# Kernel tuning notes

Hardware: AMD Instinct MI355X
Metric: run time of the kernel (lower is better)

## Reference

```python
import jax, jax.numpy as jnp
import numpy as np

N_NODES = 50000
N_EDGES = 1280000
N_GRAPHS = 64
IN_CH = 6
HID = 64
SLOPE = 0.2  # LeakyReLU negative slope


def _lrelu(x):
    return jax.nn.leaky_relu(x, SLOPE)


def _edge_conv(x, src, dst, W1, b1, W2, b2):
    # PyG EdgeConv: message = nn([x_i, x_j - x_i]); x_i = x[dst], x_j = x[src]; max-aggr onto dst
    xi = x[dst]                                   # [E, F]
    m = jnp.concatenate([xi, x[src] - xi], -1)    # [E, 2F]
    h = _lrelu(_lrelu(m @ W1 + b1) @ W2 + b2)     # [E, H]
    agg = jax.ops.segment_max(h, dst, num_segments=N_NODES)
    return jnp.where(jnp.isneginf(agg), 0.0, agg)  # nodes with no in-edges -> 0


def setup_inputs() -> dict:
    key = jax.random.key(0)
    ks = jax.random.split(key, 12)
    glorot = lambda k, fi, fo: jax.random.normal(k, (fi, fo), jnp.float32) * np.sqrt(2.0 / (fi + fo))
    x = jax.random.normal(ks[0], (N_NODES, IN_CH), jnp.float32)
    edge_index = jax.random.randint(ks[1], (2, N_EDGES), 0, N_NODES, jnp.int64 if jax.config.x64_enabled else jnp.int32)
    batch = jnp.sort(jax.random.randint(ks[2], (N_NODES,), 0, N_GRAPHS))
    return {
        "x": x, "edge_index": edge_index, "batch": batch,
        "W1": glorot(ks[3], 2 * IN_CH, HID), "b1": jnp.zeros((HID,), jnp.float32),
        "W2": glorot(ks[4], HID, HID),       "b2": jnp.zeros((HID,), jnp.float32),
        "W3": glorot(ks[5], 2 * HID, HID),   "b3": jnp.zeros((HID,), jnp.float32),
        "W4": glorot(ks[6], HID, HID),       "b4": jnp.zeros((HID,), jnp.float32),
        "Wc1": glorot(ks[7], 2 * HID, HID),  "bc1": jnp.zeros((HID,), jnp.float32),
        "Wc2": glorot(ks[8], HID, 1),        "bc2": jnp.zeros((1,), jnp.float32),
    }


def reference(x, edge_index, batch, W1, b1, W2, b2, W3, b3, W4, b4, Wc1, bc1, Wc2, bc2):
    src, dst = edge_index[0], edge_index[1]
    h = _edge_conv(x, src, dst, W1, b1, W2, b2)   # [N, H]
    h = _edge_conv(h, src, dst, W3, b3, W4, b4)   # [N, H]
    # global mean + max pool per graph
    cnt = jax.ops.segment_sum(jnp.ones((N_NODES,), h.dtype), batch, num_segments=N_GRAPHS)
    mean_p = jax.ops.segment_sum(h, batch, num_segments=N_GRAPHS) / jnp.clip(cnt, 1.0)[:, None]
    max_p = jax.ops.segment_max(h, batch, num_segments=N_GRAPHS)
    max_p = jnp.where(jnp.isneginf(max_p), 0.0, max_p)
    g = jnp.concatenate([mean_p, max_p], -1)      # [G, 2H]
    logits = _lrelu(g @ Wc1 + bc1) @ Wc2 + bc2    # dropout is identity at inference
    return logits.squeeze(-1)                      # [G]
```

## Files before the change

### kernel.cpp

```cpp
#include <hip/hip_runtime.h>
#include <hip/hip_bf16.h>

#define SLOPE 0.2f
#define NPB 64
#define CAP 2048
#define SUBCAP 384
#define MAXBUCK 1024
#define EPB 4096
#define XF1B 512
#define PPARTS 16

typedef _Float16 f16x8  __attribute__((ext_vector_type(8)));
typedef float    f32x4  __attribute__((ext_vector_type(4)));
typedef unsigned u32;
typedef unsigned u32x4  __attribute__((ext_vector_type(4)));

__device__ __forceinline__ float lrelu(float v) { return fmaxf(v, SLOPE * v); }

__device__ __forceinline__ f16x8 lrelu8(f16x8 v) {
    f16x8 s = v * (_Float16)SLOPE;
#if __has_builtin(__builtin_elementwise_max)
    return __builtin_elementwise_max(v, s);
#else
    f16x8 r;
#pragma unroll
    for (int i = 0; i < 8; ++i) r[i] = v[i] > s[i] ? v[i] : s[i];
    return r;
#endif
}

__device__ __forceinline__ void split_f16(float v, _Float16& h, _Float16& l) {
    h = (_Float16)v;
    l = (_Float16)(v - (float)h);
}
__device__ __forceinline__ u32 pack_f16(_Float16 a, _Float16 b) {
    return (u32)__builtin_bit_cast(unsigned short, a) |
           ((u32)__builtin_bit_cast(unsigned short, b) << 16);
}

__global__ void __launch_bounds__(256) scatter_xform1_kernel(
    const int* __restrict__ srcI, const int* __restrict__ dstI,
    int* __restrict__ cursor, u32* __restrict__ pairW,
    int E, int nNodes, int nBuck, int nCntB,
    const float* __restrict__ x,
    const float* __restrict__ W1, const float* __restrict__ b1,
    _Float16* __restrict__ Ph, _Float16* __restrict__ Qh)
{
    if (blockIdx.x < nCntB) {
        __shared__ int cnt4[4][MAXBUCK];
        __shared__ int base[MAXBUCK];
        const int tid = threadIdx.x;
        const int wv  = tid >> 6;
        const int j   = blockIdx.x & 7;
        const int e0 = blockIdx.x * EPB;
        const int e1 = min(e0 + EPB, E);
        const int n4 = (e1 - e0) >> 2;
        const int4* d4 = (const int4*)(dstI + e0);
        const int4* s4 = (const int4*)(srcI + e0);

        for (int b = tid; b < nBuck; b += 256) {
            cnt4[0][b] = 0; cnt4[1][b] = 0; cnt4[2][b] = 0; cnt4[3][b] = 0;
        }
        __syncthreads();
        int* mycnt = cnt4[wv];
        for (int i = tid; i < n4; i += 256) {
            const int4 d = d4[i];
            atomicAdd(&mycnt[d.x >> 6], 1);
            atomicAdd(&mycnt[d.y >> 6], 1);
            atomicAdd(&mycnt[d.z >> 6], 1);
            atomicAdd(&mycnt[d.w >> 6], 1);
        }
        for (int e = e0 + (n4 << 2) + tid; e < e1; e += 256)
            atomicAdd(&mycnt[dstI[e] >> 6], 1);
        __syncthreads();
        for (int b = tid; b < nBuck; b += 256) {
            const int c = (cnt4[0][b] + cnt4[1][b]) + (cnt4[2][b] + cnt4[3][b]);
            base[b] = (c > 0)
                ? ((b * 8 + j) * SUBCAP + min(atomicAdd(&cursor[b * 8 + j], c), SUBCAP))
                : 0;
        }
        __syncthreads();
        for (int b = tid; b < nBuck; b += 256) cnt4[0][b] = 0;
        __syncthreads();
        int* scnt = cnt4[0];
        for (int i = tid; i < n4; i += 256) {
            const int4 d = d4[i];
            const int4 s = s4[i];
            {
                const int b = d.x >> 6;
                const int loc = atomicAdd(&scnt[b], 1);
                pairW[min(base[b] + loc, (b * 8 + j + 1) * SUBCAP - 1)] =
                    ((u32)s.x << 6) | (u32)(d.x & (NPB - 1));
            }
            {
                const int b = d.y >> 6;
                const int loc = atomicAdd(&scnt[b], 1);
                pairW[min(base[b] + loc, (b * 8 + j + 1) * SUBCAP - 1)] =
                    ((u32)s.y << 6) | (u32)(d.y & (NPB - 1));
            }
            {
                const int b = d.z >> 6;
                const int loc = atomicAdd(&scnt[b], 1);
                pairW[min(base[b] + loc, (b * 8 + j + 1) * SUBCAP - 1)] =
                    ((u32)s.z << 6) | (u32)(d.z & (NPB - 1));
            }
            {
                const int b = d.w >> 6;
                const int loc = atomicAdd(&scnt[b], 1);
                pairW[min(base[b] + loc, (b * 8 + j + 1) * SUBCAP - 1)] =
                    ((u32)s.w << 6) | (u32)(d.w & (NPB - 1));
            }
        }
        for (int e = e0 + (n4 << 2) + tid; e < e1; e += 256) {
            const int d = dstI[e];
            const int b = d >> 6;
            const int loc = atomicAdd(&scnt[b], 1);
            pairW[min(base[b] + loc, (b * 8 + j + 1) * SUBCAP - 1)] =
                ((u32)srcI[e] << 6) | (u32)(d & (NPB - 1));
        }
        return;
    }
    const int lane = threadIdx.x & 63;
    const int wave = ((blockIdx.x - nCntB) * 256 + threadIdx.x) >> 6;
    const int nw   = (XF1B * 256) >> 6;

    float wd[6], wb[6];
#pragma unroll
    for (int r = 0; r < 6; ++r) {
        wb[r] = W1[(6 + r) * 64 + lane];
        wd[r] = W1[r * 64 + lane] - wb[r];
    }
    const float bb = b1[lane];
    for (int i = wave; i < nNodes; i += nw) {
        const float* xr = x + (size_t)i * 6;
        float p = bb, q = 0.f;
#pragma unroll
        for (int r = 0; r < 6; ++r) {
            float xv = xr[r];
            p = fmaf(xv, wd[r], p);
            q = fmaf(xv, wb[r], q);
        }
        Ph[(size_t)i * 64 + lane] = (_Float16)p;
        Qh[(size_t)i * 64 + lane] = (_Float16)q;
    }
}

__global__ void __launch_bounds__(256) bucket_sort_kernel(
    const u32* __restrict__ pairW, const int* __restrict__ cursor,
    int2* __restrict__ rowInfo, int* __restrict__ sortedSrc,
    int* __restrict__ fixedSrc, int nNodes)
{
    __shared__ u32 pairLds[CAP];
    __shared__ u32 sortLds[CAP];
    __shared__ int nodeCnt4[4][NPB];
    __shared__ int nodeCur4[4][NPB];
    __shared__ int nodeSt[NPB];
    __shared__ int nodeDg[NPB];
    __shared__ int wcS[8];
    __shared__ int wBase[9];
    const int b   = blockIdx.x;
    const int n0  = b * NPB;
    const int n1  = min(n0 + NPB, nNodes);
    const int tid = threadIdx.x;
    const int wv  = tid >> 6;

    if (tid < NPB) {
        nodeCnt4[0][tid] = 0; nodeCnt4[1][tid] = 0;
        nodeCnt4[2][tid] = 0; nodeCnt4[3][tid] = 0;
    }
    if (tid < 8) wcS[tid] = min(cursor[b * 8 + tid], SUBCAP);
    __syncthreads();
    if (tid == 0) {
        int acc = 0;
#pragma unroll
        for (int jj = 0; jj < 8; ++jj) { wBase[jj] = acc; acc += wcS[jj]; }
        wBase[8] = acc;
    }
    __syncthreads();

#pragma unroll
    for (int jj = 0; jj < 8; ++jj) {
        const int w0 = (b * 8 + jj) * SUBCAP;
        const int wc = wcS[jj];
        const int d0 = wBase[jj];
        const int nv = wc >> 2;
        const u32x4* p4 = (const u32x4*)(pairW + w0);
        for (int i = tid; i < nv; i += 256) {
            const u32x4 v = p4[i];
            pairLds[d0 + i * 4 + 0] = v[0];
            pairLds[d0 + i * 4 + 1] = v[1];
            pairLds[d0 + i * 4 + 2] = v[2];
            pairLds[d0 + i * 4 + 3] = v[3];
        }
        for (int i = (nv << 2) + tid; i < wc; i += 256)
            pairLds[d0 + i] = pairW[w0 + i];
    }
    __syncthreads();

    const int total = wBase[8];
    for (int i = tid; i < total; i += 256)
        atomicAdd(&nodeCnt4[wv][pairLds[i] & (NPB - 1)], 1);
    __syncthreads();
    if (tid < 64) {
        const int c0 = nodeCnt4[0][tid], c1 = nodeCnt4[1][tid];
        const int c2 = nodeCnt4[2][tid], c3 = nodeCnt4[3][tid];
        const int c = (c0 + c1) + (c2 + c3);
        int inc = c;
#pragma unroll
        for (int off = 1; off < 64; off <<= 1) {
            int t = __shfl_up(inc, off);
            if (tid >= off) inc += t;
        }
        const int stl = inc - c;
        nodeSt[tid] = stl;
        nodeDg[tid] = c;
        nodeCur4[0][tid] = stl;
        nodeCur4[1][tid] = stl + c0;
        nodeCur4[2][tid] = stl + c0 + c1;
        nodeCur4[3][tid] = stl + c0 + c1 + c2;
        if (tid < n1 - n0) rowInfo[n0 + tid] = make_int2(b * CAP + stl, c);
    }
    __syncthreads();
    for (int i = tid; i < total; i += 256) {
        const u32 w = pairLds[i];
        const int pos = atomicAdd(&nodeCur4[wv][w & (NPB - 1)], 1);
        sortLds[pos] = w >> 6;
    }
    __syncthreads();
    for (int i = tid; i < total; i += 256)
        sortedSrc[b * CAP + i] = (int)sortLds[i];
    const int nValid = n1 - n0;
    for (int idx = tid; idx < NPB * 32; idx += 256) {
        const int r = idx >> 5;
        const int i = idx & 31;
        if (r < nValid) {
            const int dg = nodeDg[r];
            const u32 v = (dg > 0) ? sortLds[nodeSt[r] + min(i, dg - 1)]
                                   : (u32)(n0 + r);
            fixedSrc[(size_t)(n0 + r) * 32 + i] = (int)v;
        }
    }
}

__global__ void __launch_bounds__(256) node_xform2_mfma_kernel(
    const _Float16* __restrict__ B1h,
    const float* __restrict__ W3, const float* __restrict__ b3,
    _Float16* __restrict__ Ph, _Float16* __restrict__ Qh, int nNodes)
{
    __shared__ u32x4 wlds[32][64];

    const int tid  = threadIdx.x;
    const int lane = tid & 63;
    const int cn   = lane & 15;
    const int q    = lane >> 4;
    const int wv   = tid >> 6;
    const int wave = (blockIdx.x * 256 + tid) >> 6;
    const int nw   = (gridDim.x * 256) >> 6;

#pragma unroll
    for (int i = 0; i < 8; ++i) {
        const int f    = wv + i * 4;
        const int isLo = f >> 4;
        const int g    = f & 15;
        const int nt   = g >> 1;
        const int ks   = g & 1;
        const int col  = (nt & 3) * 16 + cn;
        u32x4 d;
#pragma unroll
        for (int p = 0; p < 4; ++p) {
            const int k0 = ks * 32 + q * 8 + 2 * p;
            float w0, w1;
            if (nt < 4) {
                w0 = W3[k0 * 64 + col]       - W3[(64 + k0) * 64 + col];
                w1 = W3[(k0 + 1) * 64 + col] - W3[(64 + k0 + 1) * 64 + col];
            } else {
                w0 = W3[(64 + k0) * 64 + col];
                w1 = W3[(64 + k0 + 1) * 64 + col];
            }
            _Float16 h0, l0, h1, l1;
            split_f16(w0, h0, l0);
            split_f16(w1, h1, l1);
            d[p] = isLo ? pack_f16(l0, l1) : pack_f16(h0, h1);
        }
        wlds[f][lane] = d;
    }
    float bcv[4];
#pragma unroll
    for (int nt = 0; nt < 4; ++nt) bcv[nt] = b3[nt * 16 + cn];
    __syncthreads();

    const int nGrp = (nNodes + 15) >> 4;
    for (int t = wave; t < nGrp; t += nw) {
        const int n0 = t << 4;
        const int rA = min(n0 + cn, nNodes - 1);
        const f16x8* Arow = (const f16x8*)(B1h + (size_t)rA * 64);
        const f16x8 A0 = Arow[q];
        const f16x8 A1 = Arow[4 + q];

        f32x4 acc0, acc1, acc2, acc3, acc4, acc5, acc6, acc7;
#define NT_TILE(ACC, NT, INI)                                                  \
        {                                                                      \
            const f16x8 wh0 = __builtin_bit_cast(f16x8, wlds[(NT) * 2][lane]); \
            const f16x8 wh1 = __builtin_bit_cast(f16x8, wlds[(NT) * 2 + 1][lane]); \
            const f16x8 wl0 = __builtin_bit_cast(f16x8, wlds[16 + (NT) * 2][lane]); \
            const f16x8 wl1 = __builtin_bit_cast(f16x8, wlds[16 + (NT) * 2 + 1][lane]); \
            f32x4 a_; a_[0] = a_[1] = a_[2] = a_[3] = (INI);                   \
            a_ = __builtin_amdgcn_mfma_f32_16x16x32_f16(A0, wl0, a_, 0, 0, 0); \
            a_ = __builtin_amdgcn_mfma_f32_16x16x32_f16(A0, wh0, a_, 0, 0, 0); \
            a_ = __builtin_amdgcn_mfma_f32_16x16x32_f16(A1, wl1, a_, 0, 0, 0); \
            a_ = __builtin_amdgcn_mfma_f32_16x16x32_f16(A1, wh1, a_, 0, 0, 0); \
            ACC = a_;                                                          \
        }
        NT_TILE(acc0, 0, bcv[0]); NT_TILE(acc1, 1, bcv[1]);
        NT_TILE(acc2, 2, bcv[2]); NT_TILE(acc3, 3, bcv[3]);
        NT_TILE(acc4, 4, 0.0f);   NT_TILE(acc5, 5, 0.0f);
        NT_TILE(acc6, 6, 0.0f);   NT_TILE(acc7, 7, 0.0f);
#undef NT_TILE

        const int rowLim = nNodes - n0;
#pragma unroll
        for (int j = 0; j < 4; ++j) {
            const int r = 4 * q + j;
            if (r < rowLim) {
                _Float16* Pr = Ph + (size_t)(n0 + r) * 64;
                _Float16* Qr = Qh + (size_t)(n0 + r) * 64;
                Pr[cn]      = (_Float16)acc0[j];
                Pr[16 + cn] = (_Float16)acc1[j];
                Pr[32 + cn] = (_Float16)acc2[j];
                Pr[48 + cn] = (_Float16)acc3[j];
                Qr[cn]      = (_Float16)acc4[j];
                Qr[16 + cn] = (_Float16)acc5[j];
                Qr[32 + cn] = (_Float16)acc6[j];
                Qr[48 + cn] = (_Float16)acc7[j];
            }
        }
    }
}

__global__ void __launch_bounds__(256) edge_agg_mfma_kernel(
    const _Float16* __restrict__ Ph, const _Float16* __restrict__ Qh,
    const int2* __restrict__ rowInfo, const int* __restrict__ sortedSrc,
    const int* __restrict__ fixedSrc,
    const float* __restrict__ W, const float* __restrict__ b,
    _Float16* __restrict__ outB, int nNodes)
{
    __shared__ u32x4 wlds[16][64];

    const int tid  = threadIdx.x;
    const int lane = tid & 63;
    const int cn   = lane & 15;
    const int q    = lane >> 4;
    const int wv   = tid >> 6;
    const int wave = (blockIdx.x * 256 + tid) >> 6;
    const int nw   = (gridDim.x * 256) >> 6;

#pragma unroll
    for (int i = 0; i < 4; ++i) {
        const int f    = wv + i * 4;
        const int isLo = f >> 3;
        const int g    = f & 7;
        const int nt   = g >> 1;
        const int ks   = g & 1;
        u32x4 d;
#pragma unroll
        for (int p = 0; p < 4; ++p) {
            float w0 = W[(ks * 32 + q * 8 + 2 * p)     * 64 + nt * 16 + cn];
            float w1 = W[(ks * 32 + q * 8 + 2 * p + 1) * 64 + nt * 16 + cn];
            _Float16 h0, l0, h1, l1;
            split_f16(w0, h0, l0);
            split_f16(w1, h1, l1);
            d[p] = isLo ? pack_f16(l0, l1) : pack_f16(h0, h1);
        }
        wlds[f][lane] = d;
    }
    float bc[4];
#pragma unroll
    for (int nt = 0; nt < 4; ++nt) bc[nt] = b[nt * 16 + cn];
    __syncthreads();

    const u32 nClamp = (u32)(nNodes - 1);
    const int nLastN = nNodes - 1;
    const int nPairs = (nNodes + 1) >> 1;

    for (int t = wave; t < nPairs; t += nw) {
        const int n1 = 2 * t;
        const int n2 = 2 * t + 1;
        const bool has2 = (n2 < nNodes);

        const int2 ri1 = rowInfo[n1];
        const int2 ri2 = has2 ? rowInfo[n2] : make_int2(ri1.x, 0);
        const size_t fb1 = (size_t)n1 * 32;
        const size_t fb2 = (size_t)(has2 ? n2 : n1) * 32;
        u32 sA1 = (u32)fixedSrc[fb1 + cn];
        u32 sB1 = (u32)fixedSrc[fb1 + 16 + cn];
        u32 sA2 = (u32)fixedSrc[fb2 + cn];
        u32 sB2 = (u32)fixedSrc[fb2 + 16 + cn];
        sA1 = min(sA1, nClamp); sB1 = min(sB1, nClamp);
        sA2 = min(sA2, nClamp); sB2 = min(sB2, nClamp);

        const f16x8* P1 = (const f16x8*)(Ph + (size_t)n1 * 64);
        const f16x8* P2 = (const f16x8*)(Ph + (size_t)(has2 ? n2 : n1) * 64);
        const f16x8 p1A = P1[q], p1B = P1[4 + q];
        const f16x8 p2A = P2[q], p2B = P2[4 + q];

        const f16x8* QA1 = (const f16x8*)(Qh + (size_t)sA1 * 64);
        const f16x8* QB1 = (const f16x8*)(Qh + (size_t)sB1 * 64);
        const f16x8* QA2 = (const f16x8*)(Qh + (size_t)sA2 * 64);
        const f16x8* QB2 = (const f16x8*)(Qh + (size_t)sB2 * 64);
        const f16x8 qA1a = QA1[q], qA1b = QA1[4 + q];
        const f16x8 qB1a = QB1[q], qB1b = QB1[4 + q];
        const f16x8 qA2a = QA2[q], qA2b = QA2[4 + q];
        const f16x8 qB2a = QB2[q], qB2b = QB2[4 + q];

        const int rs1  = __builtin_amdgcn_readfirstlane(ri1.x);
        const int deg1 = __builtin_amdgcn_readfirstlane(ri1.y);
        const int rs2  = __builtin_amdgcn_readfirstlane(ri2.x);
        const int deg2 = __builtin_amdgcn_readfirstlane(ri2.y);
        const int d1c = max(deg1, 1) - 1;
        const int d2c = max(deg2, 1) - 1;

        float m10 = -INFINITY, m11 = -INFINITY, m12 = -INFINITY, m13 = -INFINITY;
        float m20 = -INFINITY, m21 = -INFINITY, m22 = -INFINITY, m23 = -INFINITY;

        if (deg1 > 0) {
            const f16x8 A00 = lrelu8(p1A + qA1a);
            const f16x8 A01 = lrelu8(p1B + qA1b);
            const f16x8 A10 = lrelu8(p1A + qB1a);
            const f16x8 A11 = lrelu8(p1B + qB1b);
#pragma unroll
            for (int nt = 0; nt < 4; ++nt) {
                const f16x8 wh0 = __builtin_bit_cast(f16x8, wlds[nt * 2][lane]);
                const f16x8 wh1 = __builtin_bit_cast(f16x8, wlds[nt * 2 + 1][lane]);
                const f16x8 wl0 = __builtin_bit_cast(f16x8, wlds[8 + nt * 2][lane]);
                const f16x8 wl1 = __builtin_bit_cast(f16x8, wlds[8 + nt * 2 + 1][lane]);
                f32x4 a; a[0] = a[1] = a[2] = a[3] = bc[nt];
                a = __builtin_amdgcn_mfma_f32_16x16x32_f16(A00, wl0, a, 0, 0, 0);
                a = __builtin_amdgcn_mfma_f32_16x16x32_f16(A00, wh0, a, 0, 0, 0);
                a = __builtin_amdgcn_mfma_f32_16x16x32_f16(A01, wl1, a, 0, 0, 0);
                a = __builtin_amdgcn_mfma_f32_16x16x32_f16(A01, wh1, a, 0, 0, 0);
                f32x4 c; c[0] = c[1] = c[2] = c[3] = bc[nt];
                c = __builtin_amdgcn_mfma_f32_16x16x32_f16(A10, wl0, c, 0, 0, 0);
                c = __builtin_amdgcn_mfma_f32_16x16x32_f16(A10, wh0, c, 0, 0, 0);
                c = __builtin_amdgcn_mfma_f32_16x16x32_f16(A11, wl1, c, 0, 0, 0);
                c = __builtin_amdgcn_mfma_f32_16x16x32_f16(A11, wh1, c, 0, 0, 0);
                float m = (nt == 0) ? m10 : (nt == 1) ? m11 : (nt == 2) ? m12 : m13;
                m = fmaxf(m, fmaxf(fmaxf(a[0], a[1]), fmaxf(a[2], a[3])));
                m = fmaxf(m, fmaxf(fmaxf(c[0], c[1]), fmaxf(c[2], c[3])));
                if (nt == 0) m10 = m; else if (nt == 1) m11 = m;
                else if (nt == 2) m12 = m; else m13 = m;
            }
        }
        if (deg2 > 0) {
            const f16x8 A00 = lrelu8(p2A + qA2a);
            const f16x8 A01 = lrelu8(p2B + qA2b);
            const f16x8 A10 = lrelu8(p2A + qB2a);
            const f16x8 A11 = lrelu8(p2B + qB2b);
#pragma unroll
            for (int nt = 0; nt < 4; ++nt) {
                const f16x8 wh0 = __builtin_bit_cast(f16x8, wlds[nt * 2][lane]);
                const f16x8 wh1 = __builtin_bit_cast(f16x8, wlds[nt * 2 + 1][lane]);
                const f16x8 wl0 = __builtin_bit_cast(f16x8, wlds[8 + nt * 2][lane]);
                const f16x8 wl1 = __builtin_bit_cast(f16x8, wlds[8 + nt * 2 + 1][lane]);
                f32x4 a; a[0] = a[1] = a[2] = a[3] = bc[nt];
                a = __builtin_amdgcn_mfma_f32_16x16x32_f16(A00, wl0, a, 0, 0, 0);
                a = __builtin_amdgcn_mfma_f32_16x16x32_f16(A00, wh0, a, 0, 0, 0);
                a = __builtin_amdgcn_mfma_f32_16x16x32_f16(A01, wl1, a, 0, 0, 0);
                a = __builtin_amdgcn_mfma_f32_16x16x32_f16(A01, wh1, a, 0, 0, 0);
                f32x4 c; c[0] = c[1] = c[2] = c[3] = bc[nt];
                c = __builtin_amdgcn_mfma_f32_16x16x32_f16(A10, wl0, c, 0, 0, 0);
                c = __builtin_amdgcn_mfma_f32_16x16x32_f16(A10, wh0, c, 0, 0, 0);
                c = __builtin_amdgcn_mfma_f32_16x16x32_f16(A11, wl1, c, 0, 0, 0);
                c = __builtin_amdgcn_mfma_f32_16x16x32_f16(A11, wh1, c, 0, 0, 0);
                float m = (nt == 0) ? m20 : (nt == 1) ? m21 : (nt == 2) ? m22 : m23;
                m = fmaxf(m, fmaxf(fmaxf(a[0], a[1]), fmaxf(a[2], a[3])));
                m = fmaxf(m, fmaxf(fmaxf(c[0], c[1]), fmaxf(c[2], c[3])));
                if (nt == 0) m20 = m; else if (nt == 1) m21 = m;
                else if (nt == 2) m22 = m; else m23 = m;
            }
        }

        const int gmax = max(deg1, deg2);
        for (int g0 = 32; g0 < gmax; g0 += 32) {
            u32 eA1 = (u32)sortedSrc[rs1 + min(g0 + cn,      d1c)];
            u32 eB1 = (u32)sortedSrc[rs1 + min(g0 + 16 + cn, d1c)];
            u32 eA2 = (u32)sortedSrc[rs2 + min(g0 + cn,      d2c)];
            u32 eB2 = (u32)sortedSrc[rs2 + min(g0 + 16 + cn, d2c)];
            eA1 = min(eA1, nClamp); eB1 = min(eB1, nClamp);
            eA2 = min(eA2, nClamp); eB2 = min(eB2, nClamp);
            const f16x8* EA1 = (const f16x8*)(Qh + (size_t)eA1 * 64);
            const f16x8* EB1 = (const f16x8*)(Qh + (size_t)eB1 * 64);
            const f16x8* EA2 = (const f16x8*)(Qh + (size_t)eA2 * 64);
            const f16x8* EB2 = (const f16x8*)(Qh + (size_t)eB2 * 64);
            const f16x8 gA1a = EA1[q], gA1b = EA1[4 + q];
            const f16x8 gB1a = EB1[q], gB1b = EB1[4 + q];
            const f16x8 gA2a = EA2[q], gA2b = EA2[4 + q];
            const f16x8 gB2a = EB2[q], gB2b = EB2[4 + q];

            if (g0 < deg1) {
                const f16x8 A00 = lrelu8(p1A + gA1a);
                const f16x8 A01 = lrelu8(p1B + gA1b);
                const f16x8 A10 = lrelu8(p1A + gB1a);
                const f16x8 A11 = lrelu8(p1B + gB1b);
#pragma unroll
                for (int nt = 0; nt < 4; ++nt) {
                    const f16x8 wh0 = __builtin_bit_cast(f16x8, wlds[nt * 2][lane]);
                    const f16x8 wh1 = __builtin_bit_cast(f16x8, wlds[nt * 2 + 1][lane]);
                    const f16x8 wl0 = __builtin_bit_cast(f16x8, wlds[8 + nt * 2][lane]);
                    const f16x8 wl1 = __builtin_bit_cast(f16x8, wlds[8 + nt * 2 + 1][lane]);
                    f32x4 a; a[0] = a[1] = a[2] = a[3] = bc[nt];
                    a = __builtin_amdgcn_mfma_f32_16x16x32_f16(A00, wl0, a, 0, 0, 0);
                    a = __builtin_amdgcn_mfma_f32_16x16x32_f16(A00, wh0, a, 0, 0, 0);
                    a = __builtin_amdgcn_mfma_f32_16x16x32_f16(A01, wl1, a, 0, 0, 0);
                    a = __builtin_amdgcn_mfma_f32_16x16x32_f16(A01, wh1, a, 0, 0, 0);
                    f32x4 c; c[0] = c[1] = c[2] = c[3] = bc[nt];
                    c = __builtin_amdgcn_mfma_f32_16x16x32_f16(A10, wl0, c, 0, 0, 0);
                    c = __builtin_amdgcn_mfma_f32_16x16x32_f16(A10, wh0, c, 0, 0, 0);
                    c = __builtin_amdgcn_mfma_f32_16x16x32_f16(A11, wl1, c, 0, 0, 0);
                    c = __builtin_amdgcn_mfma_f32_16x16x32_f16(A11, wh1, c, 0, 0, 0);
                    float m = (nt == 0) ? m10 : (nt == 1) ? m11 : (nt == 2) ? m12 : m13;
                    m = fmaxf(m, fmaxf(fmaxf(a[0], a[1]), fmaxf(a[2], a[3])));
                    m = fmaxf(m, fmaxf(fmaxf(c[0], c[1]), fmaxf(c[2], c[3])));
                    if (nt == 0) m10 = m; else if (nt == 1) m11 = m;
                    else if (nt == 2) m12 = m; else m13 = m;
                }
            }
            if (g0 < deg2) {
                const f16x8 A00 = lrelu8(p2A + gA2a);
                const f16x8 A01 = lrelu8(p2B + gA2b);
                const f16x8 A10 = lrelu8(p2A + gB2a);
                const f16x8 A11 = lrelu8(p2B + gB2b);
#pragma unroll
                for (int nt = 0; nt < 4; ++nt) {
                    const f16x8 wh0 = __builtin_bit_cast(f16x8, wlds[nt * 2][lane]);
                    const f16x8 wh1 = __builtin_bit_cast(f16x8, wlds[nt * 2 + 1][lane]);
                    const f16x8 wl0 = __builtin_bit_cast(f16x8, wlds[8 + nt * 2][lane]);
                    const f16x8 wl1 = __builtin_bit_cast(f16x8, wlds[8 + nt * 2 + 1][lane]);
                    f32x4 a; a[0] = a[1] = a[2] = a[3] = bc[nt];
                    a = __builtin_amdgcn_mfma_f32_16x16x32_f16(A00, wl0, a, 0, 0, 0);
                    a = __builtin_amdgcn_mfma_f32_16x16x32_f16(A00, wh0, a, 0, 0, 0);
                    a = __builtin_amdgcn_mfma_f32_16x16x32_f16(A01, wl1, a, 0, 0, 0);
                    a = __builtin_amdgcn_mfma_f32_16x16x32_f16(A01, wh1, a, 0, 0, 0);
                    f32x4 c; c[0] = c[1] = c[2] = c[3] = bc[nt];
                    c = __builtin_amdgcn_mfma_f32_16x16x32_f16(A10, wl0, c, 0, 0, 0);
                    c = __builtin_amdgcn_mfma_f32_16x16x32_f16(A10, wh0, c, 0, 0, 0);
                    c = __builtin_amdgcn_mfma_f32_16x16x32_f16(A11, wl1, c, 0, 0, 0);
                    c = __builtin_amdgcn_mfma_f32_16x16x32_f16(A11, wh1, c, 0, 0, 0);
                    float m = (nt == 0) ? m20 : (nt == 1) ? m21 : (nt == 2) ? m22 : m23;
                    m = fmaxf(m, fmaxf(fmaxf(a[0], a[1]), fmaxf(a[2], a[3])));
                    m = fmaxf(m, fmaxf(fmaxf(c[0], c[1]), fmaxf(c[2], c[3])));
                    if (nt == 0) m20 = m; else if (nt == 1) m21 = m;
                    else if (nt == 2) m22 = m; else m23 = m;
                }
            }
        }

        m10 = fmaxf(m10, __shfl_xor(m10, 16)); m10 = fmaxf(m10, __shfl_xor(m10, 32));
        m11 = fmaxf(m11, __shfl_xor(m11, 16)); m11 = fmaxf(m11, __shfl_xor(m11, 32));
        m12 = fmaxf(m12, __shfl_xor(m12, 16)); m12 = fmaxf(m12, __shfl_xor(m12, 32));
        m13 = fmaxf(m13, __shfl_xor(m13, 16)); m13 = fmaxf(m13, __shfl_xor(m13, 32));
        float sel1 = (q < 2) ? ((q == 0) ? m10 : m11) : ((q == 2) ? m12 : m13);
        outB[(size_t)n1 * 64 + q * 16 + cn] =
            (_Float16)((deg1 > 0) ? lrelu(sel1) : 0.0f);

        if (has2) {
            m20 = fmaxf(m20, __shfl_xor(m20, 16)); m20 = fmaxf(m20, __shfl_xor(m20, 32));
            m21 = fmaxf(m21, __shfl_xor(m21, 16)); m21 = fmaxf(m21, __shfl_xor(m21, 32));
            m22 = fmaxf(m22, __shfl_xor(m22, 16)); m22 = fmaxf(m22, __shfl_xor(m22, 32));
            m23 = fmaxf(m23, __shfl_xor(m23, 16)); m23 = fmaxf(m23, __shfl_xor(m23, 32));
            float sel2 = (q < 2) ? ((q == 0) ? m20 : m21) : ((q == 2) ? m22 : m23);
            outB[(size_t)n2 * 64 + q * 16 + cn] =
                (_Float16)((deg2 > 0) ? lrelu(sel2) : 0.0f);
        }
    }
}

__device__ __forceinline__ int lower_bound_i(const int* __restrict__ a, int n, int key)
{
    int lo = 0, hi = n;
    while (lo < hi) {
        int mid = (lo + hi) >> 1;
        if (a[mid] < key) lo = mid + 1; else hi = mid;
    }
    return lo;
}

__global__ void __launch_bounds__(256) pool_kernel(
    const _Float16* __restrict__ Bh, const int* __restrict__ batch,
    float* __restrict__ gpart, int nNodes)
{
    const int gid  = blockIdx.x / PPARTS;
    const int part = blockIdx.x % PPARTS;
    const int c    = threadIdx.x & 63;
    const int wid  = threadIdx.x >> 6;

    const int s = lower_bound_i(batch, nNodes, gid);
    const int e = lower_bound_i(batch, nNodes, gid + 1);
    const int len = e - s;
    const int ps = s + (len * part) / PPARTS;
    const int pe = s + (len * (part + 1)) / PPARTS;

    float sum = 0.f, mx = -INFINITY;
    for (int n = ps + wid; n < pe; n += 4) {
        float v = (float)Bh[(size_t)n * 64 + c];
        sum += v;
        mx = fmaxf(mx, v);
    }
    __shared__ float ssum[4][64];
    __shared__ float smax[4][64];
    ssum[wid][c] = sum;
    smax[wid][c] = mx;
    __syncthreads();
    if (wid == 0) {
        sum = (ssum[0][c] + ssum[1][c]) + (ssum[2][c] + ssum[3][c]);
        mx  = fmaxf(fmaxf(smax[0][c], smax[1][c]), fmaxf(smax[2][c], smax[3][c]));
        float* row = gpart + (size_t)blockIdx.x * 132;
        row[c]      = sum;
        row[64 + c] = mx;
        if (c == 0) row[128] = (float)(pe - ps);
    }
}

__global__ void __launch_bounds__(64) cls_kernel(
    const float* __restrict__ gpart,
    const float* __restrict__ Wc1, const float* __restrict__ bc1,
    const float* __restrict__ Wc2, const float* __restrict__ bc2,
    float* __restrict__ out)
{
    __shared__ float g[128];
    const int gid = blockIdx.x;
    const int c   = threadIdx.x;

    float s = 0.f, m = -INFINITY, cnt = 0.f;
#pragma unroll
    for (int p = 0; p < PPARTS; ++p) {
        const float* row = gpart + (size_t)(gid * PPARTS + p) * 132;
        s += row[c];
        m = fmaxf(m, row[64 + c]);
        cnt += row[128];
    }
    g[c]      = s / fmaxf(cnt, 1.0f);
    g[64 + c] = (cnt > 0.f) ? m : 0.0f;
    __syncthreads();

    float t = bc1[c];
#pragma unroll 8
    for (int k = 0; k < 128; ++k) t = fmaf(g[k], Wc1[k * 64 + c], t);
    t = lrelu(t);
    float p = t * Wc2[c];
#pragma unroll
    for (int off = 32; off > 0; off >>= 1) p += __shfl_down(p, off);
    if (c == 0) out[gid] = p + bc2[0];
}

static inline size_t align_up(size_t v, size_t a) { return (v + a - 1) & ~(a - 1); }

extern "C" void kernel_launch(void* const* d_in, const int* in_sizes, int n_in,
                              void* d_out, int out_size, void* d_ws, size_t ws_size,
                              hipStream_t stream)
{
    const float* x     = (const float*)d_in[0];
    const int*   ei    = (const int*)d_in[1];
    const int*   batch = (const int*)d_in[2];
    const float* W1  = (const float*)d_in[3];
    const float* b1  = (const float*)d_in[4];
    const float* W2  = (const float*)d_in[5];
    const float* b2  = (const float*)d_in[6];
    const float* W3  = (const float*)d_in[7];
    const float* b3  = (const float*)d_in[8];
    const float* W4  = (const float*)d_in[9];
    const float* b4  = (const float*)d_in[10];
    const float* Wc1 = (const float*)d_in[11];
    const float* bc1 = (const float*)d_in[12];
    const float* Wc2 = (const float*)d_in[13];
    const float* bc2 = (const float*)d_in[14];
    float* out = (float*)d_out;

    const int nNodes  = in_sizes[0] / 6;
    const int E       = in_sizes[1] / 2;
    const int nGraphs = out_size;
    const int* srcI = ei;
    const int* dstI = ei + E;
    const int nBuck = (nNodes + NPB - 1) / NPB;
    const int nCntB = (E + EPB - 1) / EPB;

    char* wsp = (char*)d_ws;
    size_t off = 0;
    int*  cursor    = (int*)(wsp + off);   off = align_up(off + (size_t)MAXBUCK * 8 * 4, 256);
    int2* rowInfo   = (int2*)(wsp + off);  off = align_up(off + (size_t)nNodes * 8, 256);
    int*  sortedSrc = (int*)(wsp + off);   off = align_up(off + (size_t)nBuck * CAP * 4, 256);
    int*  fixedSrc  = (int*)(wsp + off);   off = align_up(off + (size_t)nNodes * 32 * 4, 256);
    u32*  pairW     = (u32*)(wsp + off);   off = align_up(off + (size_t)nBuck * 8 * SUBCAP * 4, 256);
    const size_t nFeat = (size_t)nNodes * 64;
    _Float16* Ph   = (_Float16*)(wsp + off);  off = align_up(off + nFeat * 2, 256);
    _Float16* Qh   = (_Float16*)(wsp + off);  off = align_up(off + nFeat * 2, 256);
    _Float16* B1h  = (_Float16*)(wsp + off);  off = align_up(off + nFeat * 2, 256);
    _Float16* B2h  = (_Float16*)(wsp + off);  off = align_up(off + nFeat * 2, 256);
    float*    gpart= (float*)(wsp + off);     off = align_up(off + (size_t)nGraphs * PPARTS * 132 * 4, 256);
    (void)ws_size;

    (void)hipMemsetAsync(cursor, 0, (size_t)nBuck * 8 * 4, stream);
    scatter_xform1_kernel<<<nCntB + XF1B, 256, 0, stream>>>(
        srcI, dstI, cursor, pairW, E, nNodes, nBuck, nCntB, x, W1, b1, Ph, Qh);
    bucket_sort_kernel<<<nBuck, 256, 0, stream>>>(pairW, cursor, rowInfo,
                                                  sortedSrc, fixedSrc, nNodes);

    edge_agg_mfma_kernel<<<2048, 256, 0, stream>>>(Ph, Qh, rowInfo, sortedSrc,
                                                   fixedSrc, W2, b2, B1h, nNodes);
    const int nGrp   = (nNodes + 15) >> 4;
    const int xf2Blk = (nGrp + 3) >> 2;
    node_xform2_mfma_kernel<<<xf2Blk, 256, 0, stream>>>(B1h, W3, b3, Ph, Qh,
                                                        nNodes);
    edge_agg_mfma_kernel<<<2048, 256, 0, stream>>>(Ph, Qh, rowInfo, sortedSrc,
                                                   fixedSrc, W4, b4, B2h, nNodes);

    pool_kernel<<<nGraphs * PPARTS, 256, 0, stream>>>(B2h, batch, gpart, nNodes);
    cls_kernel<<<nGraphs, 64, 0, stream>>>(gpart, Wc1, bc1, Wc2, bc2, out);
}
```

Baseline: 260.9 us.

## Stage xform2 outputs through LDS and give agg waves contiguous node-pair chunks

node_xform2 now writes its P/Q tiles into per-wave LDS staging buffers and then stores full 16-byte vectors per row, replacing scattered 2-byte global stores. The edge aggregation kernel switches from a grid-stride loop with 2048 blocks to contiguous chunks of about three node pairs per wave, with the grid sized to match. The max reduction is also reassociated to shorten the dependency chain. The aim is better store coalescing, better locality in the sorted neighbour data, and higher ILP, at the cost of more blocks and extra LDS use in xform2.

```diff
diff --git a/kernel.cpp b/kernel.cpp
--- a/kernel.cpp
+++ b/kernel.cpp
@@ -248,6 +248,8 @@
     _Float16* __restrict__ Ph, _Float16* __restrict__ Qh, int nNodes)
 {
     __shared__ u32x4 wlds[32][64];
+    __shared__ _Float16 stP[4][16][64];
+    __shared__ _Float16 stQ[4][16][64];
 
     const int tid  = threadIdx.x;
     const int lane = tid & 63;
@@ -317,22 +319,28 @@
         NT_TILE(acc6, 6, 0.0f);   NT_TILE(acc7, 7, 0.0f);
 #undef NT_TILE
 
-        const int rowLim = nNodes - n0;
 #pragma unroll
         for (int j = 0; j < 4; ++j) {
             const int r = 4 * q + j;
-            if (r < rowLim) {
-                _Float16* Pr = Ph + (size_t)(n0 + r) * 64;
-                _Float16* Qr = Qh + (size_t)(n0 + r) * 64;
-                Pr[cn]      = (_Float16)acc0[j];
-                Pr[16 + cn] = (_Float16)acc1[j];
-                Pr[32 + cn] = (_Float16)acc2[j];
-                Pr[48 + cn] = (_Float16)acc3[j];
-                Qr[cn]      = (_Float16)acc4[j];
-                Qr[16 + cn] = (_Float16)acc5[j];
-                Qr[32 + cn] = (_Float16)acc6[j];
-                Qr[48 + cn] = (_Float16)acc7[j];
-            }
+            stP[wv][r][cn]      = (_Float16)acc0[j];
+            stP[wv][r][16 + cn] = (_Float16)acc1[j];
+            stP[wv][r][32 + cn] = (_Float16)acc2[j];
+            stP[wv][r][48 + cn] = (_Float16)acc3[j];
+            stQ[wv][r][cn]      = (_Float16)acc4[j];
+            stQ[wv][r][16 + cn] = (_Float16)acc5[j];
+            stQ[wv][r][32 + cn] = (_Float16)acc6[j];
+            stQ[wv][r][48 + cn] = (_Float16)acc7[j];
+        }
+        const int rowLim = nNodes - n0;
+        const int rr = lane >> 2;
+        const int c0 = (lane & 3) * 16;
+        if (rr < rowLim) {
+            const f16x8* sp = (const f16x8*)&stP[wv][rr][c0];
+            const f16x8* sq = (const f16x8*)&stQ[wv][rr][c0];
+            f16x8* gp = (f16x8*)(Ph + (size_t)(n0 + rr) * 64 + c0);
+            f16x8* gq = (f16x8*)(Qh + (size_t)(n0 + rr) * 64 + c0);
+            gp[0] = sp[0]; gp[1] = sp[1];
+            gq[0] = sq[0]; gq[1] = sq[1];
         }
     }
 }
@@ -382,7 +390,11 @@
     const int nLastN = nNodes - 1;
     const int nPairs = (nNodes + 1) >> 1;
 
-    for (int t = wave; t < nPairs; t += nw) {
+    const int C    = (nPairs + nw - 1) / nw;
+    const int tBeg = wave * C;
+    const int tEnd = min(tBeg + C, nPairs);
+
+    for (int t = tBeg; t < tEnd; ++t) {
         const int n1 = 2 * t;
         const int n2 = 2 * t + 1;
         const bool has2 = (n2 < nNodes);
@@ -444,8 +456,10 @@
                 c = __builtin_amdgcn_mfma_f32_16x16x32_f16(A11, wl1, c, 0, 0, 0);
                 c = __builtin_amdgcn_mfma_f32_16x16x32_f16(A11, wh1, c, 0, 0, 0);
                 float m = (nt == 0) ? m10 : (nt == 1) ? m11 : (nt == 2) ? m12 : m13;
-                m = fmaxf(m, fmaxf(fmaxf(a[0], a[1]), fmaxf(a[2], a[3])));
-                m = fmaxf(m, fmaxf(fmaxf(c[0], c[1]), fmaxf(c[2], c[3])));
+                const float u1 = fmaxf(fmaxf(a[0], a[1]), a[2]);
+                const float u2 = fmaxf(fmaxf(a[3], c[0]), c[1]);
+                const float u3 = fmaxf(fmaxf(c[2], c[3]), m);
+                m = fmaxf(fmaxf(u1, u2), u3);
                 if (nt == 0) m10 = m; else if (nt == 1) m11 = m;
                 else if (nt == 2) m12 = m; else m13 = m;
             }
@@ -472,8 +486,10 @@
                 c = __builtin_amdgcn_mfma_f32_16x16x32_f16(A11, wl1, c, 0, 0, 0);
                 c = __builtin_amdgcn_mfma_f32_16x16x32_f16(A11, wh1, c, 0, 0, 0);
                 float m = (nt == 0) ? m20 : (nt == 1) ? m21 : (nt == 2) ? m22 : m23;
-                m = fmaxf(m, fmaxf(fmaxf(a[0], a[1]), fmaxf(a[2], a[3])));
-                m = fmaxf(m, fmaxf(fmaxf(c[0], c[1]), fmaxf(c[2], c[3])));
+                const float u1 = fmaxf(fmaxf(a[0], a[1]), a[2]);
+                const float u2 = fmaxf(fmaxf(a[3], c[0]), c[1]);
+                const float u3 = fmaxf(fmaxf(c[2], c[3]), m);
+                m = fmaxf(fmaxf(u1, u2), u3);
                 if (nt == 0) m20 = m; else if (nt == 1) m21 = m;
                 else if (nt == 2) m22 = m; else m23 = m;
             }
@@ -518,8 +534,10 @@
                     c = __builtin_amdgcn_mfma_f32_16x16x32_f16(A11, wl1, c, 0, 0, 0);
                     c = __builtin_amdgcn_mfma_f32_16x16x32_f16(A11, wh1, c, 0, 0, 0);
                     float m = (nt == 0) ? m10 : (nt == 1) ? m11 : (nt == 2) ? m12 : m13;
-                    m = fmaxf(m, fmaxf(fmaxf(a[0], a[1]), fmaxf(a[2], a[3])));
-                    m = fmaxf(m, fmaxf(fmaxf(c[0], c[1]), fmaxf(c[2], c[3])));
+                    const float u1 = fmaxf(fmaxf(a[0], a[1]), a[2]);
+                    const float u2 = fmaxf(fmaxf(a[3], c[0]), c[1]);
+                    const float u3 = fmaxf(fmaxf(c[2], c[3]), m);
+                    m = fmaxf(fmaxf(u1, u2), u3);
                     if (nt == 0) m10 = m; else if (nt == 1) m11 = m;
                     else if (nt == 2) m12 = m; else m13 = m;
                 }
@@ -546,8 +564,10 @@
                     c = __builtin_amdgcn_mfma_f32_16x16x32_f16(A11, wl1, c, 0, 0, 0);
                     c = __builtin_amdgcn_mfma_f32_16x16x32_f16(A11, wh1, c, 0, 0, 0);
                     float m = (nt == 0) ? m20 : (nt == 1) ? m21 : (nt == 2) ? m22 : m23;
-                    m = fmaxf(m, fmaxf(fmaxf(a[0], a[1]), fmaxf(a[2], a[3])));
-                    m = fmaxf(m, fmaxf(fmaxf(c[0], c[1]), fmaxf(c[2], c[3])));
+                    const float u1 = fmaxf(fmaxf(a[0], a[1]), a[2]);
+                    const float u2 = fmaxf(fmaxf(a[3], c[0]), c[1]);
+                    const float u3 = fmaxf(fmaxf(c[2], c[3]), m);
+                    m = fmaxf(fmaxf(u1, u2), u3);
                     if (nt == 0) m20 = m; else if (nt == 1) m21 = m;
                     else if (nt == 2) m22 = m; else m23 = m;
                 }
@@ -704,14 +724,18 @@
     bucket_sort_kernel<<<nBuck, 256, 0, stream>>>(pairW, cursor, rowInfo,
                                                   sortedSrc, fixedSrc, nNodes);
 
-    edge_agg_mfma_kernel<<<2048, 256, 0, stream>>>(Ph, Qh, rowInfo, sortedSrc,
-                                                   fixedSrc, W2, b2, B1h, nNodes);
+    const int nPairs    = (nNodes + 1) / 2;
+    const int aggWaves  = (nPairs + 2) / 3;
+    const int aggBlocks = (aggWaves + 3) / 4 > 0 ? (aggWaves + 3) / 4 : 1;
+
+    edge_agg_mfma_kernel<<<aggBlocks, 256, 0, stream>>>(Ph, Qh, rowInfo, sortedSrc,
+                                                        fixedSrc, W2, b2, B1h, nNodes);
     const int nGrp   = (nNodes + 15) >> 4;
     const int xf2Blk = (nGrp + 3) >> 2;
     node_xform2_mfma_kernel<<<xf2Blk, 256, 0, stream>>>(B1h, W3, b3, Ph, Qh,
                                                         nNodes);
-    edge_agg_mfma_kernel<<<2048, 256, 0, stream>>>(Ph, Qh, rowInfo, sortedSrc,
-                                                   fixedSrc, W4, b4, B2h, nNodes);
+    edge_agg_mfma_kernel<<<aggBlocks, 256, 0, stream>>>(Ph, Qh, rowInfo, sortedSrc,
+                                                        fixedSrc, W4, b4, B2h, nNodes);
 
     pool_kernel<<<nGraphs * PPARTS, 256, 0, stream>>>(B2h, batch, gpart, nNodes);
     cls_kernel<<<nGraphs, 64, 0, stream>>>(gpart, Wc1, bc1, Wc2, bc2, out);
```

New measurement: 262.2 us. About the same (+0.5%).

## Merge build/sort and pool/classifier kernels via cooperative grid sync

Applied to the files above, without the earlier changes.

Fuses the scatter+xform1 kernel with the bucket sort kernel, and the pool kernel with the classifier kernel. Each pair becomes one cooperative launch that uses a grid-wide barrier instead of a kernel boundary. The goal is to remove launch overhead and inter-kernel gaps for the small kernels. The build kernel puts its two shared-memory layouts in a union, so per-block LDS use may change. Cooperative launch needs every block (nCntB+XF1B, about 825) resident at once, which could limit occupancy or make the launch fail.

```diff
diff --git a/kernel.cpp b/kernel.cpp
--- a/kernel.cpp
+++ b/kernel.cpp
@@ -1,5 +1,8 @@
 #include <hip/hip_runtime.h>
 #include <hip/hip_bf16.h>
+#include <hip/hip_cooperative_groups.h>
+
+namespace cg = cooperative_groups;
 
 #define SLOPE 0.2f
 #define NPB 64
@@ -38,19 +41,32 @@
            ((u32)__builtin_bit_cast(unsigned short, b) << 16);
 }
 
-__global__ void __launch_bounds__(256) scatter_xform1_kernel(
+__global__ void __launch_bounds__(256) build_kernel(
     const int* __restrict__ srcI, const int* __restrict__ dstI,
     int* __restrict__ cursor, u32* __restrict__ pairW,
     int E, int nNodes, int nBuck, int nCntB,
     const float* __restrict__ x,
     const float* __restrict__ W1, const float* __restrict__ b1,
-    _Float16* __restrict__ Ph, _Float16* __restrict__ Qh)
+    _Float16* __restrict__ Ph, _Float16* __restrict__ Qh,
+    int2* __restrict__ rowInfo, int* __restrict__ sortedSrc,
+    int* __restrict__ fixedSrc)
 {
-    if (blockIdx.x < nCntB) {
-        __shared__ int cnt4[4][MAXBUCK];
-        __shared__ int base[MAXBUCK];
-        const int tid = threadIdx.x;
-        const int wv  = tid >> 6;
+    __shared__ union {
+        struct { int cnt4[4][MAXBUCK]; int base[MAXBUCK]; } sc;
+        struct {
+            u32 pairLds[CAP]; u32 sortLds[CAP];
+            int nodeCnt4[4][NPB]; int nodeCur4[4][NPB];
+            int nodeSt[NPB]; int nodeDg[NPB];
+            int wcS[8]; int wBase[9];
+        } bk;
+    } u;
+
+    const int tid = threadIdx.x;
+    const int wv  = tid >> 6;
+
+    if (blockIdx.x < (unsigned)nCntB) {
+        int (*cnt4)[MAXBUCK] = u.sc.cnt4;
+        int* base = u.sc.base;
         const int j   = blockIdx.x & 7;
         const int e0 = blockIdx.x * EPB;
         const int e1 = min(e0 + EPB, E);
@@ -118,126 +134,123 @@
             pairW[min(base[b] + loc, (b * 8 + j + 1) * SUBCAP - 1)] =
                 ((u32)srcI[e] << 6) | (u32)(d & (NPB - 1));
         }
-        return;
-    }
-    const int lane = threadIdx.x & 63;
-    const int wave = ((blockIdx.x - nCntB) * 256 + threadIdx.x) >> 6;
-    const int nw   = (XF1B * 256) >> 6;
-
-    float wd[6], wb[6];
-#pragma unroll
-    for (int r = 0; r < 6; ++r) {
-        wb[r] = W1[(6 + r) * 64 + lane];
-        wd[r] = W1[r * 64 + lane] - wb[r];
-    }
-    const float bb = b1[lane];
-    for (int i = wave; i < nNodes; i += nw) {
-        const float* xr = x + (size_t)i * 6;
-        float p = bb, q = 0.f;
+    } else if (blockIdx.x < (unsigned)(nCntB + XF1B)) {
+        const int lane = tid & 63;
+        const int wave = ((blockIdx.x - nCntB) * 256 + tid) >> 6;
+        const int nw   = (XF1B * 256) >> 6;
+
+        float wd[6], wb[6];
 #pragma unroll
         for (int r = 0; r < 6; ++r) {
-            float xv = xr[r];
-            p = fmaf(xv, wd[r], p);
-            q = fmaf(xv, wb[r], q);
-        }
-        Ph[(size_t)i * 64 + lane] = (_Float16)p;
-        Qh[(size_t)i * 64 + lane] = (_Float16)q;
-    }
-}
-
-__global__ void __launch_bounds__(256) bucket_sort_kernel(
-    const u32* __restrict__ pairW, const int* __restrict__ cursor,
-    int2* __restrict__ rowInfo, int* __restrict__ sortedSrc,
-    int* __restrict__ fixedSrc, int nNodes)
-{
-    __shared__ u32 pairLds[CAP];
-    __shared__ u32 sortLds[CAP];
-    __shared__ int nodeCnt4[4][NPB];
-    __shared__ int nodeCur4[4][NPB];
-    __shared__ int nodeSt[NPB];
-    __shared__ int nodeDg[NPB];
-    __shared__ int wcS[8];
-    __shared__ int wBase[9];
-    const int b   = blockIdx.x;
-    const int n0  = b * NPB;
-    const int n1  = min(n0 + NPB, nNodes);
-    const int tid = threadIdx.x;
-    const int wv  = tid >> 6;
-
-    if (tid < NPB) {
-        nodeCnt4[0][tid] = 0; nodeCnt4[1][tid] = 0;
-        nodeCnt4[2][tid] = 0; nodeCnt4[3][tid] = 0;
-    }
-    if (tid < 8) wcS[tid] = min(cursor[b * 8 + tid], SUBCAP);
-    __syncthreads();
-    if (tid == 0) {
-        int acc = 0;
-#pragma unroll
-        for (int jj = 0; jj < 8; ++jj) { wBase[jj] = acc; acc += wcS[jj]; }
-        wBase[8] = acc;
-    }
-    __syncthreads();
-
-#pragma unroll
-    for (int jj = 0; jj < 8; ++jj) {
-        const int w0 = (b * 8 + jj) * SUBCAP;
-        const int wc = wcS[jj];
-        const int d0 = wBase[jj];
-        const int nv = wc >> 2;
-        const u32x4* p4 = (const u32x4*)(pairW + w0);
-        for (int i = tid; i < nv; i += 256) {
-            const u32x4 v = p4[i];
-            pairLds[d0 + i * 4 + 0] = v[0];
-            pairLds[d0 + i * 4 + 1] = v[1];
-            pairLds[d0 + i * 4 + 2] = v[2];
-            pairLds[d0 + i * 4 + 3] = v[3];
-        }
-        for (int i = (nv << 2) + tid; i < wc; i += 256)
-            pairLds[d0 + i] = pairW[w0 + i];
-    }
-    __syncthreads();
-
-    const int total = wBase[8];
-    for (int i = tid; i < total; i += 256)
-        atomicAdd(&nodeCnt4[wv][pairLds[i] & (NPB - 1)], 1);
-    __syncthreads();
-    if (tid < 64) {
-        const int c0 = nodeCnt4[0][tid], c1 = nodeCnt4[1][tid];
-        const int c2 = nodeCnt4[2][tid], c3 = nodeCnt4[3][tid];
-        const int c = (c0 + c1) + (c2 + c3);
-        int inc = c;
-#pragma unroll
-        for (int off = 1; off < 64; off <<= 1) {
-            int t = __shfl_up(inc, off);
-            if (tid >= off) inc += t;
-        }
-        const int stl = inc - c;
-        nodeSt[tid] = stl;
-        nodeDg[tid] = c;
-        nodeCur4[0][tid] = stl;
-        nodeCur4[1][tid] = stl + c0;
-        nodeCur4[2][tid] = stl + c0 + c1;
-        nodeCur4[3][tid] = stl + c0 + c1 + c2;
-        if (tid < n1 - n0) rowInfo[n0 + tid] = make_int2(b * CAP + stl, c);
-    }
-    __syncthreads();
-    for (int i = tid; i < total; i += 256) {
-        const u32 w = pairLds[i];
-        const int pos = atomicAdd(&nodeCur4[wv][w & (NPB - 1)], 1);
-        sortLds[pos] = w >> 6;
-    }
-    __syncthreads();
-    for (int i = tid; i < total; i += 256)
-        sortedSrc[b * CAP + i] = (int)sortLds[i];
-    const int nValid = n1 - n0;
-    for (int idx = tid; idx < NPB * 32; idx += 256) {
-        const int r = idx >> 5;
-        const int i = idx & 31;
-        if (r < nValid) {
-            const int dg = nodeDg[r];
-            const u32 v = (dg > 0) ? sortLds[nodeSt[r] + min(i, dg - 1)]
-                                   : (u32)(n0 + r);
-            fixedSrc[(size_t)(n0 + r) * 32 + i] = (int)v;
+            wb[r] = W1[(6 + r) * 64 + lane];
+            wd[r] = W1[r * 64 + lane] - wb[r];
+        }
+        const float bb = b1[lane];
+        for (int i = wave; i < nNodes; i += nw) {
+            const float* xr = x + (size_t)i * 6;
+            float p = bb, q = 0.f;
+#pragma unroll
+            for (int r = 0; r < 6; ++r) {
+                float xv = xr[r];
+                p = fmaf(xv, wd[r], p);
+                q = fmaf(xv, wb[r], q);
+            }
+            Ph[(size_t)i * 64 + lane] = (_Float16)p;
+            Qh[(size_t)i * 64 + lane] = (_Float16)q;
+        }
+    }
+
+    cg::this_grid().sync();
+
+    if (blockIdx.x < (unsigned)nBuck) {
+        u32* pairLds = u.bk.pairLds;
+        u32* sortLds = u.bk.sortLds;
+        int (*nodeCnt4)[NPB] = u.bk.nodeCnt4;
+        int (*nodeCur4)[NPB] = u.bk.nodeCur4;
+        int* nodeSt = u.bk.nodeSt;
+        int* nodeDg = u.bk.nodeDg;
+        int* wcS    = u.bk.wcS;
+        int* wBase  = u.bk.wBase;
+
+        const int b   = blockIdx.x;
+        const int n0  = b * NPB;
+        const int n1  = min(n0 + NPB, nNodes);
+
+        if (tid < NPB) {
+            nodeCnt4[0][tid] = 0; nodeCnt4[1][tid] = 0;
+            nodeCnt4[2][tid] = 0; nodeCnt4[3][tid] = 0;
+        }
+        if (tid < 8) wcS[tid] = min(cursor[b * 8 + tid], SUBCAP);
+        __syncthreads();
+        if (tid == 0) {
+            int acc = 0;
+#pragma unroll
+            for (int jj = 0; jj < 8; ++jj) { wBase[jj] = acc; acc += wcS[jj]; }
+            wBase[8] = acc;
+        }
+        __syncthreads();
+
+#pragma unroll
+        for (int jj = 0; jj < 8; ++jj) {
+            const int w0 = (b * 8 + jj) * SUBCAP;
+            const int wc = wcS[jj];
+            const int d0 = wBase[jj];
+            const int nv = wc >> 2;
+            const u32x4* p4 = (const u32x4*)(pairW + w0);
+            for (int i = tid; i < nv; i += 256) {
+                const u32x4 v = p4[i];
+                pairLds[d0 + i * 4 + 0] = v[0];
+                pairLds[d0 + i * 4 + 1] = v[1];
+                pairLds[d0 + i * 4 + 2] = v[2];
+                pairLds[d0 + i * 4 + 3] = v[3];
+            }
+            for (int i = (nv << 2) + tid; i < wc; i += 256)
+                pairLds[d0 + i] = pairW[w0 + i];
+        }
+        __syncthreads();
+
+        const int total = wBase[8];
+        for (int i = tid; i < total; i += 256)
+            atomicAdd(&nodeCnt4[wv][pairLds[i] & (NPB - 1)], 1);
+        __syncthreads();
+        if (tid < 64) {
+            const int c0 = nodeCnt4[0][tid], c1 = nodeCnt4[1][tid];
+            const int c2 = nodeCnt4[2][tid], c3 = nodeCnt4[3][tid];
+            const int c = (c0 + c1) + (c2 + c3);
+            int inc = c;
+#pragma unroll
+            for (int off = 1; off < 64; off <<= 1) {
+                int t = __shfl_up(inc, off);
+                if (tid >= off) inc += t;
+            }
+            const int stl = inc - c;
+            nodeSt[tid] = stl;
+            nodeDg[tid] = c;
+            nodeCur4[0][tid] = stl;
+            nodeCur4[1][tid] = stl + c0;
+            nodeCur4[2][tid] = stl + c0 + c1;
+            nodeCur4[3][tid] = stl + c0 + c1 + c2;
+            if (tid < n1 - n0) rowInfo[n0 + tid] = make_int2(b * CAP + stl, c);
+        }
+        __syncthreads();
+        for (int i = tid; i < total; i += 256) {
+            const u32 w = pairLds[i];
+            const int pos = atomicAdd(&nodeCur4[wv][w & (NPB - 1)], 1);
+            sortLds[pos] = w >> 6;
+        }
+        __syncthreads();
+        for (int i = tid; i < total; i += 256)
+            sortedSrc[b * CAP + i] = (int)sortLds[i];
+        const int nValid = n1 - n0;
+        for (int idx = tid; idx < NPB * 32; idx += 256) {
+            const int r = idx >> 5;
+            const int i = idx & 31;
+            if (r < nValid) {
+                const int dg = nodeDg[r];
+                const u32 v = (dg > 0) ? sortLds[nodeSt[r] + min(i, dg - 1)]
+                                       : (u32)(n0 + r);
+                fixedSrc[(size_t)(n0 + r) * 32 + i] = (int)v;
+            }
         }
     }
 }
@@ -584,72 +597,78 @@
     return lo;
 }
 
-__global__ void __launch_bounds__(256) pool_kernel(
+__global__ void __launch_bounds__(256) pool_cls_kernel(
     const _Float16* __restrict__ Bh, const int* __restrict__ batch,
-    float* __restrict__ gpart, int nNodes)
+    float* __restrict__ gpart,
+    const float* __restrict__ Wc1, const float* __restrict__ bc1,
+    const float* __restrict__ Wc2, const float* __restrict__ bc2,
+    float* __restrict__ out, int nNodes, int nGraphs)
 {
-    const int gid  = blockIdx.x / PPARTS;
-    const int part = blockIdx.x % PPARTS;
-    const int c    = threadIdx.x & 63;
-    const int wid  = threadIdx.x >> 6;
-
-    const int s = lower_bound_i(batch, nNodes, gid);
-    const int e = lower_bound_i(batch, nNodes, gid + 1);
-    const int len = e - s;
-    const int ps = s + (len * part) / PPARTS;
-    const int pe = s + (len * (part + 1)) / PPARTS;
-
-    float sum = 0.f, mx = -INFINITY;
-    for (int n = ps + wid; n < pe; n += 4) {
-        float v = (float)Bh[(size_t)n * 64 + c];
-        sum += v;
-        mx = fmaxf(mx, v);
-    }
     __shared__ float ssum[4][64];
     __shared__ float smax[4][64];
-    ssum[wid][c] = sum;
-    smax[wid][c] = mx;
-    __syncthreads();
-    if (wid == 0) {
-        sum = (ssum[0][c] + ssum[1][c]) + (ssum[2][c] + ssum[3][c]);
-        mx  = fmaxf(fmaxf(smax[0][c], smax[1][c]), fmaxf(smax[2][c], smax[3][c]));
-        float* row = gpart + (size_t)blockIdx.x * 132;
-        row[c]      = sum;
-        row[64 + c] = mx;
-        if (c == 0) row[128] = (float)(pe - ps);
-    }
-}
-
-__global__ void __launch_bounds__(64) cls_kernel(
-    const float* __restrict__ gpart,
-    const float* __restrict__ Wc1, const float* __restrict__ bc1,
-    const float* __restrict__ Wc2, const float* __restrict__ bc2,
-    float* __restrict__ out)
-{
     __shared__ float g[128];
-    const int gid = blockIdx.x;
-    const int c   = threadIdx.x;
-
-    float s = 0.f, m = -INFINITY, cnt = 0.f;
-#pragma unroll
-    for (int p = 0; p < PPARTS; ++p) {
-        const float* row = gpart + (size_t)(gid * PPARTS + p) * 132;
-        s += row[c];
-        m = fmaxf(m, row[64 + c]);
-        cnt += row[128];
-    }
-    g[c]      = s / fmaxf(cnt, 1.0f);
-    g[64 + c] = (cnt > 0.f) ? m : 0.0f;
-    __syncthreads();
-
-    float t = bc1[c];
+
+    {
+        const int gid  = blockIdx.x / PPARTS;
+        const int part = blockIdx.x % PPARTS;
+        const int c    = threadIdx.x & 63;
+        const int wid  = threadIdx.x >> 6;
+
+        const int s = lower_bound_i(batch, nNodes, gid);
+        const int e = lower_bound_i(batch, nNodes, gid + 1);
+        const int len = e - s;
+        const int ps = s + (len * part) / PPARTS;
+        const int pe = s + (len * (part + 1)) / PPARTS;
+
+        float sum = 0.f, mx = -INFINITY;
+        for (int n = ps + wid; n < pe; n += 4) {
+            float v = (float)Bh[(size_t)n * 64 + c];
+            sum += v;
+            mx = fmaxf(mx, v);
+        }
+        ssum[wid][c] = sum;
+        smax[wid][c] = mx;
+        __syncthreads();
+        if (wid == 0) {
+            sum = (ssum[0][c] + ssum[1][c]) + (ssum[2][c] + ssum[3][c]);
+            mx  = fmaxf(fmaxf(smax[0][c], smax[1][c]), fmaxf(smax[2][c], smax[3][c]));
+            float* row = gpart + (size_t)blockIdx.x * 132;
+            row[c]      = sum;
+            row[64 + c] = mx;
+            if (c == 0) row[128] = (float)(pe - ps);
+        }
+    }
+
+    cg::this_grid().sync();
+
+    if (blockIdx.x < (unsigned)nGraphs) {
+        const int gid = blockIdx.x;
+        const int c   = threadIdx.x;
+
+        if (c < 64) {
+            float s = 0.f, m = -INFINITY, cnt = 0.f;
+#pragma unroll
+            for (int p = 0; p < PPARTS; ++p) {
+                const float* row = gpart + (size_t)(gid * PPARTS + p) * 132;
+                s += row[c];
+                m = fmaxf(m, row[64 + c]);
+                cnt += row[128];
+            }
+            g[c]      = s / fmaxf(cnt, 1.0f);
+            g[64 + c] = (cnt > 0.f) ? m : 0.0f;
+        }
+        __syncthreads();
+        if (c < 64) {
+            float t = bc1[c];
 #pragma unroll 8
-    for (int k = 0; k < 128; ++k) t = fmaf(g[k], Wc1[k * 64 + c], t);
-    t = lrelu(t);
-    float p = t * Wc2[c];
-#pragma unroll
-    for (int off = 32; off > 0; off >>= 1) p += __shfl_down(p, off);
-    if (c == 0) out[gid] = p + bc2[0];
+            for (int k = 0; k < 128; ++k) t = fmaf(g[k], Wc1[k * 64 + c], t);
+            t = lrelu(t);
+            float p = t * Wc2[c];
+#pragma unroll
+            for (int off = 32; off > 0; off >>= 1) p += __shfl_down(p, off);
+            if (c == 0) out[gid] = p + bc2[0];
+        }
+    }
 }
 
 static inline size_t align_up(size_t v, size_t a) { return (v + a - 1) & ~(a - 1); }
@@ -699,10 +718,24 @@
     (void)ws_size;
 
     (void)hipMemsetAsync(cursor, 0, (size_t)nBuck * 8 * 4, stream);
-    scatter_xform1_kernel<<<nCntB + XF1B, 256, 0, stream>>>(
-        srcI, dstI, cursor, pairW, E, nNodes, nBuck, nCntB, x, W1, b1, Ph, Qh);
-    bucket_sort_kernel<<<nBuck, 256, 0, stream>>>(pairW, cursor, rowInfo,
-                                                  sortedSrc, fixedSrc, nNodes);
+    {
+        int buildBlocks = nCntB + XF1B;
+        if (nBuck > buildBlocks) buildBlocks = nBuck;
+        const int* a_srcI = srcI; const int* a_dstI = dstI;
+        int* a_cursor = cursor; u32* a_pairW = pairW;
+        int a_E = E, a_nNodes = nNodes, a_nBuck = nBuck, a_nCntB = nCntB;
+        const float* a_x = x; const float* a_W1 = W1; const float* a_b1 = b1;
+        _Float16* a_Ph = Ph; _Float16* a_Qh = Qh;
+        int2* a_rowInfo = rowInfo; int* a_sortedSrc = sortedSrc;
+        int* a_fixedSrc = fixedSrc;
+        void* args[] = { &a_srcI, &a_dstI, &a_cursor, &a_pairW,
+                         &a_E, &a_nNodes, &a_nBuck, &a_nCntB,
+                         &a_x, &a_W1, &a_b1, &a_Ph, &a_Qh,
+                         &a_rowInfo, &a_sortedSrc, &a_fixedSrc };
+        (void)hipLaunchCooperativeKernel((void*)build_kernel,
+                                         dim3(buildBlocks), dim3(256),
+                                         args, 0, stream);
+    }
 
     edge_agg_mfma_kernel<<<2048, 256, 0, stream>>>(Ph, Qh, rowInfo, sortedSrc,
                                                    fixedSrc, W2, b2, B1h, nNodes);
@@ -713,6 +746,16 @@
     edge_agg_mfma_kernel<<<2048, 256, 0, stream>>>(Ph, Qh, rowInfo, sortedSrc,
                                                    fixedSrc, W4, b4, B2h, nNodes);
 
-    pool_kernel<<<nGraphs * PPARTS, 256, 0, stream>>>(B2h, batch, gpart, nNodes);
-    cls_kernel<<<nGraphs, 64, 0, stream>>>(gpart, Wc1, bc1, Wc2, bc2, out);
-}
+    {
+        const _Float16* a_Bh = B2h; const int* a_batch = batch;
+        float* a_gpart = gpart;
+        const float* a_Wc1 = Wc1; const float* a_bc1 = bc1;
+        const float* a_Wc2 = Wc2; const float* a_bc2 = bc2;
+        float* a_out = out; int a_nNodes = nNodes, a_nGraphs = nGraphs;
+        void* args[] = { &a_Bh, &a_batch, &a_gpart, &a_Wc1, &a_bc1,
+                         &a_Wc2, &a_bc2, &a_out, &a_nNodes, &a_nGraphs };
+        (void)hipLaunchCooperativeKernel((void*)pool_cls_kernel,
+                                         dim3(nGraphs * PPARTS), dim3(256),
+                                         args, 0, stream);
+    }
+}
```

Result: slower. 522.1 us (+100.2%).
